# Kernel optimization log

Measured on AMD Instinct MI355X. Metric: run time of the kernel, lower is better.

## Reference

```python
import jax, jax.numpy as jnp
import numpy as np


def setup_inputs() -> dict:
    key = jax.random.key(0)
    ks = jax.random.split(key, 8)
    B, T, D, H, HD = 4, 2048, 1024, 16, 64
    s = 0.02
    return {
        "x": jax.random.normal(ks[0], (B, T, D), dtype=jnp.float32),
        "Wq": jax.random.normal(ks[1], (H, D, HD), dtype=jnp.float32) * s,
        "bq": jnp.zeros((H, HD), dtype=jnp.float32),
        "Wk": jax.random.normal(ks[2], (H, D, HD), dtype=jnp.float32) * s,
        "bk": jnp.zeros((H, HD), dtype=jnp.float32),
        "Wv": jax.random.normal(ks[3], (H, D, HD), dtype=jnp.float32) * s,
        "bv": jnp.zeros((H, HD), dtype=jnp.float32),
        "Wo": jax.random.normal(ks[4], (D, D), dtype=jnp.float32) * s,
        "bo": jnp.zeros((D,), dtype=jnp.float32),
        "mask": 1,
    }


def reference(x, Wq, bq, Wk, bk, Wv, bv, Wo, bo, mask):
    B, T, D = x.shape
    # stacked per-head projections: [B,H,T,hd]
    q = jnp.einsum('btd,hde->bhte', x, Wq) + bq[None, :, None, :]
    k = jnp.einsum('btd,hde->bhte', x, Wk) + bk[None, :, None, :]
    v = jnp.einsum('btd,hde->bhte', x, Wv) + bv[None, :, None, :]
    hd = q.shape[-1]
    # FAITHFUL to source: scores = QK^T / hd**(-0.5) == QK^T * sqrt(hd)
    scores = jnp.einsum('bhte,bhse->bhts', q, k) * (float(hd) ** 0.5)
    if mask:
        causal = jnp.tril(jnp.ones((T, T), dtype=bool))
        scores = jnp.where(causal[None, None, :, :], scores, -jnp.inf)
    att = jax.nn.softmax(scores, axis=-1)  # dropout is identity in eval
    out = jnp.einsum('bhts,bhse->bhte', att, v)
    # concat heads along feature dim (head order matches ModuleList order)
    out = out.transpose(0, 2, 1, 3).reshape(B, T, D)
    return out @ Wo + bo
```

## Files before the change

### kernel.cpp

```cpp
#include <hip/hip_runtime.h>
#include <hip/hip_bf16.h>
#include <math.h>

#define B_  4
#define T_  2048
#define D_  1024
#define H_  16
#define HD_ 64
#define M_  8192

typedef __attribute__((ext_vector_type(8))) _Float16 f16x8;
typedef __attribute__((ext_vector_type(2))) __fp16  h16x2;
typedef __attribute__((ext_vector_type(4))) float   f32x4;

static __device__ __forceinline__ unsigned short f2h(float f){
    union { _Float16 h; unsigned short u; } cv; cv.h = (_Float16)f; return cv.u;
}
static __device__ __forceinline__ unsigned int pkh2(float a, float b){
    union { h16x2 h; unsigned int u; } cv;
    cv.h = __builtin_amdgcn_cvt_pkrtz(a, b);
    return cv.u;
}
static __device__ __forceinline__ void gload_lds16(const void* g, void* l){
    __builtin_amdgcn_global_load_lds(
        (const __attribute__((address_space(1))) unsigned int*)g,
        (__attribute__((address_space(3))) unsigned int*)l, 16, 0, 0);
}

union U16x16 { unsigned short us[16]; uint4 q[2]; };
union U16x4  { unsigned short us[4];  uint2 q;    };

__global__ __launch_bounds__(256) void prep_xh(
    const float* __restrict__ x, unsigned short* __restrict__ xb)
{
    const size_t i = ((size_t)blockIdx.x*256 + threadIdx.x)*16;
    U16x16 u;
#pragma unroll
    for (int j=0;j<16;j+=4){
        float4 f = *(const float4*)(x+i+j);
        u.us[j+0]=f2h(f.x); u.us[j+1]=f2h(f.y);
        u.us[j+2]=f2h(f.z); u.us[j+3]=f2h(f.w);
    }
    *(uint4*)(xb+i)   = u.q[0];
    *(uint4*)(xb+i+8) = u.q[1];
}

__global__ __launch_bounds__(256) void prep_wqkvh(
    const float* __restrict__ Wq, const float* __restrict__ Wk,
    const float* __restrict__ Wv, unsigned short* __restrict__ wt)
{
    const int dt = blockIdx.x;
    const int zh = blockIdx.y;
    const int z = zh >> 4, h = zh & 15;
    const float* src = ((z==0)?Wq:(z==1)?Wk:Wv) + (size_t)h*1024*64;
    __shared__ float Tt[64][68];
    const int t = threadIdx.x;
    const int r = t >> 2, c4 = (t & 3) * 16;
    const float* sp = src + (size_t)(dt*64 + r)*64 + c4;
    float4 v0=*(const float4*)(sp+0), v1=*(const float4*)(sp+4);
    float4 v2=*(const float4*)(sp+8), v3=*(const float4*)(sp+12);
    *(float4*)&Tt[r][c4+ 0]=v0; *(float4*)&Tt[r][c4+ 4]=v1;
    *(float4*)&Tt[r][c4+ 8]=v2; *(float4*)&Tt[r][c4+12]=v3;
    __syncthreads();
    const int er = t >> 2, dk = (t & 3) * 16;
    U16x16 u;
#pragma unroll
    for (int j=0;j<16;j++) u.us[j] = f2h(Tt[dk+j][er]);
    unsigned short* dst = wt + (size_t)(z*1024 + h*64 + er)*1024 + dt*64 + dk;
    *(uint4*)(dst)   = u.q[0];
    *(uint4*)(dst+8) = u.q[1];
}

__global__ __launch_bounds__(256) void prep_woh(
    const float* __restrict__ Wo, unsigned short* __restrict__ wot)
{
    const int kt = blockIdx.x, nt = blockIdx.y;
    __shared__ float Tt[64][68];
    const int t = threadIdx.x;
    const int r = t >> 2, c4 = (t & 3) * 16;
    const float* sp = Wo + (size_t)(kt*64 + r)*1024 + nt*64 + c4;
    float4 v0=*(const float4*)(sp+0), v1=*(const float4*)(sp+4);
    float4 v2=*(const float4*)(sp+8), v3=*(const float4*)(sp+12);
    *(float4*)&Tt[r][c4+ 0]=v0; *(float4*)&Tt[r][c4+ 4]=v1;
    *(float4*)&Tt[r][c4+ 8]=v2; *(float4*)&Tt[r][c4+12]=v3;
    __syncthreads();
    const int er = t >> 2, dk = (t & 3) * 16;
    U16x16 u;
#pragma unroll
    for (int j=0;j<16;j++) u.us[j] = f2h(Tt[dk+j][er]);
    unsigned short* dst = wot + (size_t)(nt*64 + er)*1024 + kt*64 + dk;
    *(uint4*)(dst)   = u.q[0];
    *(uint4*)(dst+8) = u.q[1];
}

__global__ __launch_bounds__(256) void gemm_qkvh(
    const unsigned short* __restrict__ xb, const unsigned short* __restrict__ wt,
    const float* __restrict__ bqv, const float* __restrict__ bkv,
    const float* __restrict__ bvv,
    unsigned short* __restrict__ qp, unsigned short* __restrict__ kp,
    unsigned short* __restrict__ vtp)
{
    const int m0 = blockIdx.x * 128;
    const int n0 = blockIdx.y * 128;
    const int tid = threadIdx.x;
    const int lane = tid & 63, w = tid >> 6;
    const int wr = w >> 1, wc = w & 1;
    const int fla = lane & 15, flb = lane >> 4;

    __shared__ unsigned short As[128*32];
    __shared__ unsigned short Bs[128*32];

    f32x4 acc[4][4];
#pragma unroll
    for (int i=0;i<4;i++)
#pragma unroll
        for (int j=0;j<4;j++) acc[i][j] = (f32x4){0.f,0.f,0.f,0.f};

    const int srow0 = w*32 + (lane>>2);
    const int srow1 = srow0 + 16;
    const int spc   = lane & 3;
    const size_t ga0 = (size_t)(m0+srow0)*1024 + (size_t)((spc ^ ((srow0>>1)&3))*8);
    const size_t ga1 = (size_t)(m0+srow1)*1024 + (size_t)((spc ^ ((srow1>>1)&3))*8);
    const size_t gb0 = (size_t)(n0+srow0)*1024 + (size_t)((spc ^ ((srow0>>1)&3))*8);
    const size_t gb1 = (size_t)(n0+srow1)*1024 + (size_t)((spc ^ ((srow1>>1)&3))*8);
    const int ldso0 = w*1024;
    const int ldso1 = w*1024 + 512;
    const int pchunk = (flb ^ ((fla>>1)&3)) * 8;

    for (int ks = 0; ks < 32; ++ks){
        const size_t k0 = (size_t)ks*32;
        __syncthreads();
        gload_lds16(xb + ga0 + k0, As + ldso0);
        gload_lds16(xb + ga1 + k0, As + ldso1);
        gload_lds16(wt + gb0 + k0, Bs + ldso0);
        gload_lds16(wt + gb1 + k0, Bs + ldso1);
        __syncthreads();

        f16x8 af[4], bfr[4];
#pragma unroll
        for (int mf=0; mf<4; ++mf)
            af[mf] = *(const f16x8*)&As[(wr*64+mf*16+fla)*32 + pchunk];
#pragma unroll
        for (int nf=0; nf<4; ++nf)
            bfr[nf] = *(const f16x8*)&Bs[(wc*64+nf*16+fla)*32 + pchunk];
#pragma unroll
        for (int mf=0; mf<4; ++mf)
#pragma unroll
            for (int nf=0; nf<4; ++nf)
                acc[mf][nf] = __builtin_amdgcn_mfma_f32_16x16x32_f16(
                                  af[mf], bfr[nf], acc[mf][nf], 0, 0, 0);
    }

#pragma unroll
    for (int nf=0; nf<4; ++nf){
        const int c = n0 + wc*64 + nf*16 + fla;
        const int z = c >> 10, rem = c & 1023;
        const int h = rem >> 6, e = rem & 63;
        if (z < 2){
            const float bias = ((z==0)?bqv:bkv)[rem];
            const float scl  = (z==0) ? 11.541560327111708f
                                      : 1.0f;
            unsigned short* op = (z==0)?qp:kp;
#pragma unroll
            for (int mf=0; mf<4; ++mf){
#pragma unroll
                for (int ri=0; ri<4; ++ri){
                    const int m = m0 + wr*64 + mf*16 + flb*4 + ri;
                    const int b = m >> 11, t = m & (T_-1);
                    op[((size_t)(b*H_ + h)*T_ + t)*HD_ + e] =
                        f2h((acc[mf][nf][ri] + bias) * scl);
                }
            }
        } else {
            const float bias = bvv[rem];
#pragma unroll
            for (int mf=0; mf<4; ++mf){
                const int m = m0 + wr*64 + mf*16 + flb*4;
                const int b = m >> 11, t = m & (T_-1);
                U16x4 u;
#pragma unroll
                for (int ri=0; ri<4; ++ri)
                    u.us[ri] = f2h(acc[mf][nf][ri] + bias);
                *(uint2*)(vtp + ((size_t)(b*H_ + h)*HD_ + e)*T_ + t) = u.q;
            }
        }
    }
}

__global__ __launch_bounds__(256) void gemm_o(
    const unsigned short* __restrict__ attb, const unsigned short* __restrict__ wot,
    const float* __restrict__ bo, float* __restrict__ out)
{
    const int m0 = blockIdx.x * 128;
    const int n0 = blockIdx.y * 128;
    const int tid = threadIdx.x;
    const int lane = tid & 63, w = tid >> 6;
    const int wr = w >> 1, wc = w & 1;
    const int fla = lane & 15, flb = lane >> 4;

    __shared__ unsigned short As[4096];
    __shared__ unsigned short Bs[4096];

    f32x4 acc[4][4];
#pragma unroll
    for (int i=0;i<4;i++)
#pragma unroll
        for (int j=0;j<4;j++) acc[i][j] = (f32x4){0.f,0.f,0.f,0.f};

    const int srow0 = w*32 + (lane>>2);
    const int srow1 = srow0 + 16;
    const int spc   = lane & 3;
    const size_t ga0 = (size_t)(m0+srow0)*1024 + (size_t)((spc ^ ((srow0>>1)&3))*8);
    const size_t ga1 = (size_t)(m0+srow1)*1024 + (size_t)((spc ^ ((srow1>>1)&3))*8);
    const size_t gb0 = (size_t)(n0+srow0)*1024 + (size_t)((spc ^ ((srow0>>1)&3))*8);
    const size_t gb1 = (size_t)(n0+srow1)*1024 + (size_t)((spc ^ ((srow1>>1)&3))*8);
    const int ldso0 = w*1024;
    const int ldso1 = w*1024 + 512;
    const int pchunk = (flb ^ ((fla>>1)&3)) * 8;

    for (int ks = 0; ks < 32; ++ks){
        const size_t k0 = (size_t)ks*32;
        __syncthreads();
        gload_lds16(attb + ga0 + k0, As + ldso0);
        gload_lds16(attb + ga1 + k0, As + ldso1);
        gload_lds16(wot  + gb0 + k0, Bs + ldso0);
        gload_lds16(wot  + gb1 + k0, Bs + ldso1);
        __syncthreads();

        f16x8 af[4], bfr[4];
#pragma unroll
        for (int mf=0; mf<4; ++mf)
            af[mf] = *(const f16x8*)&As[(wr*64+mf*16+fla)*32 + pchunk];
#pragma unroll
        for (int nf=0; nf<4; ++nf)
            bfr[nf] = *(const f16x8*)&Bs[(wc*64+nf*16+fla)*32 + pchunk];
#pragma unroll
        for (int mf=0; mf<4; ++mf)
#pragma unroll
            for (int nf=0; nf<4; ++nf)
                acc[mf][nf] = __builtin_amdgcn_mfma_f32_16x16x32_f16(
                                  af[mf], bfr[nf], acc[mf][nf], 0, 0, 0);
    }

#pragma unroll
    for (int nf=0; nf<4; ++nf){
        const int n = n0 + wc*64 + nf*16 + fla;
        const float bias = bo[n];
#pragma unroll
        for (int mf=0; mf<4; ++mf){
#pragma unroll
            for (int ri=0; ri<4; ++ri){
                const int m = m0 + wr*64 + mf*16 + flb*4 + ri;
                out[(size_t)m*D_ + n] = acc[mf][nf][ri] + bias;
            }
        }
    }
}

__global__ __launch_bounds__(256) void attn_mfma(
    const unsigned short* __restrict__ qp, const unsigned short* __restrict__ kp,
    const unsigned short* __restrict__ vtp, unsigned short* __restrict__ attb,
    const int* __restrict__ maskp)
{
    const int bid = blockIdx.x;
    const int qb  = 31 - (bid >> 6);
    const int bh  = bid & 63;
    const int b   = bh >> 4, h = bh & 15;
    const int tid = threadIdx.x;
    const int lane = tid & 63, w = tid >> 6;
    const int l16 = lane & 15, h16 = lane >> 4;
    const int domask = maskp[0];

    __shared__ unsigned short KPS[8192];
    __shared__ unsigned short VtS[4][64][32];

    const int qrow = qb*64 + w*16 + l16;
    const size_t qoff = ((size_t)bh*T_ + qrow)*HD_ + 8*h16;
    const f16x8 q0 = *(const f16x8*)(qp + qoff);
    const f16x8 q1 = *(const f16x8*)(qp + qoff + 32);

    f32x4 accO[4];
#pragma unroll
    for (int j=0;j<4;j++) accO[j] = (f32x4){0.f,0.f,0.f,0.f};
    float m_run = -INFINITY, lpart = 0.f;

    const int kr = tid >> 1;
    const int kh = tid & 1;
    const int fk = (kr >> 1) & 3;
    const int vr = tid >> 2;
    const int vq = tid & 3;
    const int fv = (vr >> 1) & 3;

    const int off = (h16 ^ ((l16>>1)&3)) * 8;
    const int psw = (l16>>1)&3;

    const size_t kbase = (size_t)bh*T_*HD_;
    const size_t vbase = (size_t)bh*HD_*T_;

    const int nchunks = domask ? ((qb+2)>>1) : 16;
    for (int ci = 0; ci < nchunks; ++ci){
        const int kb = ci << 7;
        const unsigned short* ksrc = kp + kbase + (size_t)(kb+kr)*HD_ + kh*32;
        uint4 ka0=*(const uint4*)(ksrc),    ka1=*(const uint4*)(ksrc+8);
        uint4 ka2=*(const uint4*)(ksrc+16), ka3=*(const uint4*)(ksrc+24);
        const unsigned short* vsrc = vtp + vbase + (size_t)vr*T_ + kb + vq*32;
        uint4 va0=*(const uint4*)(vsrc),    va1=*(const uint4*)(vsrc+8);
        uint4 va2=*(const uint4*)(vsrc+16), va3=*(const uint4*)(vsrc+24);
        __syncthreads();
        *(uint4*)&KPS[kh*4096 + kr*32 + ((0^fk)*8)] = ka0;
        *(uint4*)&KPS[kh*4096 + kr*32 + ((1^fk)*8)] = ka1;
        *(uint4*)&KPS[kh*4096 + kr*32 + ((2^fk)*8)] = ka2;
        *(uint4*)&KPS[kh*4096 + kr*32 + ((3^fk)*8)] = ka3;
        *(uint4*)&VtS[vq][vr][(0^fv)*8] = va0;
        *(uint4*)&VtS[vq][vr][(1^fv)*8] = va1;
        *(uint4*)&VtS[vq][vr][(2^fv)*8] = va2;
        *(uint4*)&VtS[vq][vr][(3^fv)*8] = va3;
        __syncthreads();

        f32x4 s[8];
#pragma unroll
        for (int j=0;j<8;j++){
            const f16x8 k0 = *(const f16x8*)&KPS[       (j*16+l16)*32 + off];
            const f16x8 k1 = *(const f16x8*)&KPS[4096 + (j*16+l16)*32 + off];
            f32x4 a = (f32x4){0.f,0.f,0.f,0.f};
            a = __builtin_amdgcn_mfma_f32_16x16x32_f16(k0, q0, a, 0,0,0);
            a = __builtin_amdgcn_mfma_f32_16x16x32_f16(k1, q1, a, 0,0,0);
            s[j] = a;
        }
        if (domask && ci == nchunks-1){
#pragma unroll
            for (int j=0;j<8;j++)
#pragma unroll
                for (int reg=0;reg<4;reg++)
                    if (kb + j*16 + 4*h16 + reg > qrow)
                        s[j][reg] = -INFINITY;
        }

        float mx01 = fmaxf(fmaxf(s[0][0],s[0][1]), fmaxf(s[0][2],s[0][3]));
        float mx1  = fmaxf(fmaxf(s[1][0],s[1][1]), fmaxf(s[1][2],s[1][3]));
        float mx2  = fmaxf(fmaxf(s[2][0],s[2][1]), fmaxf(s[2][2],s[2][3]));
        float mx3  = fmaxf(fmaxf(s[3][0],s[3][1]), fmaxf(s[3][2],s[3][3]));
        float mx4  = fmaxf(fmaxf(s[4][0],s[4][1]), fmaxf(s[4][2],s[4][3]));
        float mx5  = fmaxf(fmaxf(s[5][0],s[5][1]), fmaxf(s[5][2],s[5][3]));
        float mx6  = fmaxf(fmaxf(s[6][0],s[6][1]), fmaxf(s[6][2],s[6][3]));
        float mx7  = fmaxf(fmaxf(s[7][0],s[7][1]), fmaxf(s[7][2],s[7][3]));
        float mloc = fmaxf(fmaxf(fmaxf(mx01,mx1), fmaxf(mx2,mx3)),
                           fmaxf(fmaxf(mx4,mx5), fmaxf(mx6,mx7)));
        mloc = fmaxf(mloc, __shfl_xor(mloc,16));
        mloc = fmaxf(mloc, __shfl_xor(mloc,32));

        const bool small = (mloc <= m_run + 8.f);
        if (!__all(small)){
            const float mnew = fmaxf(m_run, mloc);
            const float scl  = exp2f(m_run - mnew);
            m_run = mnew;
            lpart *= scl;
            const float sr0 = __shfl(scl, 4*h16+0);
            const float sr1 = __shfl(scl, 4*h16+1);
            const float sr2 = __shfl(scl, 4*h16+2);
            const float sr3 = __shfl(scl, 4*h16+3);
#pragma unroll
            for (int j=0;j<4;j++){
                accO[j][0] *= sr0; accO[j][1] *= sr1;
                accO[j][2] *= sr2; accO[j][3] *= sr3;
            }
        }

        __syncthreads();

        const int prow = w*16 + l16;
        float ps = 0.f;
#pragma unroll
        for (int j=0;j<8;j++){
            const float p0 = exp2f(s[j][0]-m_run);
            const float p1 = exp2f(s[j][1]-m_run);
            const float p2 = exp2f(s[j][2]-m_run);
            const float p3 = exp2f(s[j][3]-m_run);
            ps += (p0+p1)+(p2+p3);
            const unsigned int u01 = pkh2(p0,p1);
            const unsigned int u23 = pkh2(p2,p3);
            const int sb = 2*(j&1) + (h16>>1);
            const int so = ((sb ^ psw)<<3) + 4*(h16&1);
            *(unsigned int*)&KPS[(j>>1)*2048 + prow*32 + so]     = u01;
            *(unsigned int*)&KPS[(j>>1)*2048 + prow*32 + so + 2] = u23;
        }
        lpart += ps;

#pragma unroll
        for (int kc=0;kc<4;kc++){
            const f16x8 pa = *(const f16x8*)&KPS[kc*2048 + (w*16+l16)*32 + off];
#pragma unroll
            for (int j=0;j<4;j++){
                const f16x8 vb_ = *(const f16x8*)&VtS[kc][j*16+l16][off];
                accO[j] = __builtin_amdgcn_mfma_f32_16x16x32_f16(pa, vb_, accO[j], 0,0,0);
            }
        }
    }

    float l = lpart;
    l += __shfl_xor(l,16); l += __shfl_xor(l,32);
    const float inv = 1.0f / l;
    const float ir0 = __shfl(inv, 4*h16+0);
    const float ir1 = __shfl(inv, 4*h16+1);
    const float ir2 = __shfl(inv, 4*h16+2);
    const float ir3 = __shfl(inv, 4*h16+3);
    const int t0 = qb*64 + w*16 + 4*h16;
#pragma unroll
    for (int j=0;j<4;j++){
        const size_t base = ((size_t)b*T_ + t0)*D_ + h*HD_ + j*16 + l16;
        attb[base        ] = f2h(accO[j][0]*ir0);
        attb[base +   D_ ] = f2h(accO[j][1]*ir1);
        attb[base + 2*D_ ] = f2h(accO[j][2]*ir2);
        attb[base + 3*D_ ] = f2h(accO[j][3]*ir3);
    }
}

extern "C" void kernel_launch(void* const* d_in, const int* in_sizes, int n_in,
                              void* d_out, int out_size, void* d_ws, size_t ws_size,
                              hipStream_t stream)
{
    const float* x  = (const float*)d_in[0];
    const float* Wq = (const float*)d_in[1];
    const float* bq = (const float*)d_in[2];
    const float* Wk = (const float*)d_in[3];
    const float* bk = (const float*)d_in[4];
    const float* Wv = (const float*)d_in[5];
    const float* bv = (const float*)d_in[6];
    const float* Wo = (const float*)d_in[7];
    const float* bo = (const float*)d_in[8];
    const int* mask = (const int*)d_in[9];
    float* out = (float*)d_out;

    unsigned short* qp  = (unsigned short*)d_ws;
    unsigned short* kp  = qp  + (size_t)8*1024*1024;
    unsigned short* vtp = kp  + (size_t)8*1024*1024;
    unsigned short* xb  = vtp + (size_t)8*1024*1024;
    unsigned short* wt  = xb  + (size_t)8*1024*1024;
    unsigned short* wot = wt  + (size_t)3*1024*1024;
    unsigned short* attb = xb;

    prep_xh   <<<2048, 256, 0, stream>>>(x, xb);
    prep_wqkvh<<<dim3(16,48), 256, 0, stream>>>(Wq, Wk, Wv, wt);
    prep_woh  <<<dim3(16,16), 256, 0, stream>>>(Wo, wot);
    gemm_qkvh <<<dim3(64,24), 256, 0, stream>>>(xb, wt, bq, bk, bv, qp, kp, vtp);
    attn_mfma <<<2048, 256, 0, stream>>>(qp, kp, vtp, attb, mask);
    gemm_o    <<<dim3(64,8), 256, 0, stream>>>(attb, wot, bo, out);
}
```

Baseline: 190.5 us.

## Double attention query tile to 128 rows with 512-thread blocks sharing K/V

The attention kernel now processes 128 query rows per block using 8 wavefronts instead of 64 rows with 4. Each K/V chunk loaded into shared memory is reused by twice as many queries, which halves total K/V global traffic and the number of blocks. The cooperative load is split over 512 threads, and the P staging buffer grows to 16K halves. In exchange, shared memory per block rises and causal load balance gets coarser, since the last chunk now masks over a 128-row tile. There are also fewer blocks to fill the GPU.

```diff
diff --git a/kernel.cpp b/kernel.cpp
--- a/kernel.cpp
+++ b/kernel.cpp
@@ -257,13 +257,13 @@
     }
 }
 
-__global__ __launch_bounds__(256) void attn_mfma(
+__global__ __launch_bounds__(512) void attn_mfma(
     const unsigned short* __restrict__ qp, const unsigned short* __restrict__ kp,
     const unsigned short* __restrict__ vtp, unsigned short* __restrict__ attb,
     const int* __restrict__ maskp)
 {
     const int bid = blockIdx.x;
-    const int qb  = 31 - (bid >> 6);
+    const int qb2 = 15 - (bid >> 6);
     const int bh  = bid & 63;
     const int b   = bh >> 4, h = bh & 15;
     const int tid = threadIdx.x;
@@ -271,10 +271,10 @@
     const int l16 = lane & 15, h16 = lane >> 4;
     const int domask = maskp[0];
 
-    __shared__ unsigned short KPS[8192];
+    __shared__ unsigned short KPS[16384];
     __shared__ unsigned short VtS[4][64][32];
 
-    const int qrow = qb*64 + w*16 + l16;
+    const int qrow = qb2*128 + w*16 + l16;
     const size_t qoff = ((size_t)bh*T_ + qrow)*HD_ + 8*h16;
     const f16x8 q0 = *(const f16x8*)(qp + qoff);
     const f16x8 q1 = *(const f16x8*)(qp + qoff + 32);
@@ -284,12 +284,16 @@
     for (int j=0;j<4;j++) accO[j] = (f32x4){0.f,0.f,0.f,0.f};
     float m_run = -INFINITY, lpart = 0.f;
 
-    const int kr = tid >> 1;
-    const int kh = tid & 1;
-    const int fk = (kr >> 1) & 3;
-    const int vr = tid >> 2;
-    const int vq = tid & 3;
-    const int fv = (vr >> 1) & 3;
+    const int kr  = tid >> 2;
+    const int kq  = tid & 3;
+    const int kh  = kq >> 1;
+    const int ksb = (kq & 1) * 2;
+    const int fk  = (kr >> 1) & 3;
+    const int vr  = tid >> 3;
+    const int vs8 = tid & 7;
+    const int vq  = vs8 >> 1;
+    const int vsb = (vs8 & 1) * 2;
+    const int fv  = (vr >> 1) & 3;
 
     const int off = (h16 ^ ((l16>>1)&3)) * 8;
     const int psw = (l16>>1)&3;
@@ -297,24 +301,18 @@
     const size_t kbase = (size_t)bh*T_*HD_;
     const size_t vbase = (size_t)bh*HD_*T_;
 
-    const int nchunks = domask ? ((qb+2)>>1) : 16;
+    const int nchunks = domask ? (qb2+1) : 16;
     for (int ci = 0; ci < nchunks; ++ci){
         const int kb = ci << 7;
-        const unsigned short* ksrc = kp + kbase + (size_t)(kb+kr)*HD_ + kh*32;
-        uint4 ka0=*(const uint4*)(ksrc),    ka1=*(const uint4*)(ksrc+8);
-        uint4 ka2=*(const uint4*)(ksrc+16), ka3=*(const uint4*)(ksrc+24);
-        const unsigned short* vsrc = vtp + vbase + (size_t)vr*T_ + kb + vq*32;
-        uint4 va0=*(const uint4*)(vsrc),    va1=*(const uint4*)(vsrc+8);
-        uint4 va2=*(const uint4*)(vsrc+16), va3=*(const uint4*)(vsrc+24);
-        __syncthreads();
-        *(uint4*)&KPS[kh*4096 + kr*32 + ((0^fk)*8)] = ka0;
-        *(uint4*)&KPS[kh*4096 + kr*32 + ((1^fk)*8)] = ka1;
-        *(uint4*)&KPS[kh*4096 + kr*32 + ((2^fk)*8)] = ka2;
-        *(uint4*)&KPS[kh*4096 + kr*32 + ((3^fk)*8)] = ka3;
-        *(uint4*)&VtS[vq][vr][(0^fv)*8] = va0;
-        *(uint4*)&VtS[vq][vr][(1^fv)*8] = va1;
-        *(uint4*)&VtS[vq][vr][(2^fv)*8] = va2;
-        *(uint4*)&VtS[vq][vr][(3^fv)*8] = va3;
+        const unsigned short* ksrc = kp + kbase + (size_t)(kb+kr)*HD_ + kq*16;
+        uint4 ka0=*(const uint4*)(ksrc), ka1=*(const uint4*)(ksrc+8);
+        const unsigned short* vsrc = vtp + vbase + (size_t)vr*T_ + kb + vs8*16;
+        uint4 va0=*(const uint4*)(vsrc), va1=*(const uint4*)(vsrc+8);
+        __syncthreads();
+        *(uint4*)&KPS[kh*4096 + kr*32 + (((ksb  )^fk)*8)] = ka0;
+        *(uint4*)&KPS[kh*4096 + kr*32 + (((ksb+1)^fk)*8)] = ka1;
+        *(uint4*)&VtS[vq][vr][((vsb  )^fv)*8] = va0;
+        *(uint4*)&VtS[vq][vr][((vsb+1)^fv)*8] = va1;
         __syncthreads();
 
         f32x4 s[8];
@@ -381,14 +379,14 @@
             const unsigned int u23 = pkh2(p2,p3);
             const int sb = 2*(j&1) + (h16>>1);
             const int so = ((sb ^ psw)<<3) + 4*(h16&1);
-            *(unsigned int*)&KPS[(j>>1)*2048 + prow*32 + so]     = u01;
-            *(unsigned int*)&KPS[(j>>1)*2048 + prow*32 + so + 2] = u23;
+            *(unsigned int*)&KPS[(j>>1)*4096 + prow*32 + so]     = u01;
+            *(unsigned int*)&KPS[(j>>1)*4096 + prow*32 + so + 2] = u23;
         }
         lpart += ps;
 
 #pragma unroll
         for (int kc=0;kc<4;kc++){
-            const f16x8 pa = *(const f16x8*)&KPS[kc*2048 + (w*16+l16)*32 + off];
+            const f16x8 pa = *(const f16x8*)&KPS[kc*4096 + (w*16+l16)*32 + off];
 #pragma unroll
             for (int j=0;j<4;j++){
                 const f16x8 vb_ = *(const f16x8*)&VtS[kc][j*16+l16][off];
@@ -404,7 +402,7 @@
     const float ir1 = __shfl(inv, 4*h16+1);
     const float ir2 = __shfl(inv, 4*h16+2);
     const float ir3 = __shfl(inv, 4*h16+3);
-    const int t0 = qb*64 + w*16 + 4*h16;
+    const int t0 = qb2*128 + w*16 + 4*h16;
 #pragma unroll
     for (int j=0;j<4;j++){
         const size_t base = ((size_t)b*T_ + t0)*D_ + h*HD_ + j*16 + l16;
@@ -443,6 +441,6 @@
     prep_wqkvh<<<dim3(16,48), 256, 0, stream>>>(Wq, Wk, Wv, wt);
     prep_woh  <<<dim3(16,16), 256, 0, stream>>>(Wo, wot);
     gemm_qkvh <<<dim3(64,24), 256, 0, stream>>>(xb, wt, bq, bk, bv, qp, kp, vtp);
-    attn_mfma <<<2048, 256, 0, stream>>>(qp, kp, vtp, attb, mask);
+    attn_mfma <<<1024, 512, 0, stream>>>(qp, kp, vtp, attb, mask);
     gemm_o    <<<dim3(64,8), 256, 0, stream>>>(attb, wot, bo, out);
 }
```

New measurement: 180.4 us. 1.06x faster.
